# Kernel tuning notes

Measured on AMD Instinct MI355X. Metric: run time of the kernel, lower is better.

Reference implementation:

```python
import jax, jax.numpy as jnp
import numpy as np
from jax import lax

T, B = 256, 64
VOCAB, D_EMBED, D_HIDDEN = 32000, 512, 1024


def setup_inputs() -> dict:
    key = jax.random.key(0)
    k1, k2, k3, k4 = jax.random.split(key, 4)
    x_seq = jax.random.randint(k1, (T, B), 0, VOCAB, dtype=jnp.int64) if jax.config.jax_enable_x64 else jax.random.randint(k1, (T, B), 0, VOCAB, dtype=jnp.int32)
    scale_e = 1.0
    scale_ih = 1.0 / np.sqrt(D_HIDDEN)
    return {
        "x_seq": x_seq,
        "embedding": jax.random.normal(k2, (VOCAB, D_EMBED), dtype=jnp.float32) * scale_e,
        "W_ih": jax.random.normal(k3, (4 * D_HIDDEN, D_EMBED), dtype=jnp.float32) * scale_ih,
        "W_hh": jax.random.normal(k4, (4 * D_HIDDEN, D_HIDDEN), dtype=jnp.float32) * scale_ih,
        "b_ih": jnp.zeros((4 * D_HIDDEN,), dtype=jnp.float32),
        "b_hh": jnp.zeros((4 * D_HIDDEN,), dtype=jnp.float32),
    }


def reference(x_seq, embedding, W_ih, W_hh, b_ih, b_hh):
    # e_seq: [T, B, E]
    e_seq = embedding[x_seq]
    B_ = x_seq.shape[1]
    H = W_hh.shape[1]
    # Precompute input projections for all timesteps in one big GEMM: [T, B, 4H]
    x_gates = jnp.einsum("tbe,ge->tbg", e_seq, W_ih) + b_ih + b_hh

    def step(carry, xg):
        h, c = carry
        gates = xg + h @ W_hh.T  # [B, 4H]
        i, f, g, o = jnp.split(gates, 4, axis=-1)  # PyTorch gate order i,f,g,o
        i = jax.nn.sigmoid(i)
        f = jax.nn.sigmoid(f)
        g = jnp.tanh(g)
        o = jax.nn.sigmoid(o)
        c_new = f * c + i * g
        h_new = o * jnp.tanh(c_new)
        return (h_new, c_new), h_new

    h0 = jnp.zeros((B_, H), dtype=e_seq.dtype)
    c0 = jnp.zeros((B_, H), dtype=e_seq.dtype)
    (h, c), outs = lax.scan(step, (h0, c0), x_gates)
    return outs, h, c
```

## Files before the change

kernel.cpp:

```cpp
#include <hip/hip_runtime.h>
#include <hip/hip_bf16.h>
#include <cstdint>
#include <cstddef>

#define T_STEPS 256
#define BATCH   64
#define DE      512
#define DH      1024
#define NBLK    64

typedef short  bf16x8 __attribute__((ext_vector_type(8)));
typedef float  f32x4  __attribute__((ext_vector_type(4)));
typedef unsigned long long u64;

#define LSBMASK 0x0001000100010001ull

__device__ __forceinline__ unsigned short bf_bits(__hip_bfloat16 h) {
    union { __hip_bfloat16 h; unsigned short u; } x; x.h = h; return x.u;
}
__device__ __forceinline__ float b2f(unsigned short u) {
    union { float f; unsigned v; } x; x.v = ((unsigned)u) << 16; return x.f;
}

__device__ __forceinline__ void async_copy16(const void* gsrc, void* ldst) {
    __builtin_amdgcn_global_load_lds(
        (const __attribute__((address_space(1))) unsigned int*)gsrc,
        (__attribute__((address_space(3))) unsigned int*)ldst,
        16, 0, 0);
}

__device__ __forceinline__ u64 llc_load64(const u64* p) {
    return __hip_atomic_load(p, __ATOMIC_RELAXED, __HIP_MEMORY_SCOPE_AGENT);
}
__device__ __forceinline__ void llc_store16(unsigned short* p, unsigned short v) {
    __hip_atomic_store(p, v, __ATOMIC_RELAXED, __HIP_MEMORY_SCOPE_AGENT);
}

__global__ void k_init(u64* __restrict__ hbuf) {
    int i = blockIdx.x * 256 + threadIdx.x;
    hbuf[i] = (i < 16384) ? 0ull : LSBMASK;
}

__global__ void k_f32_to_bf16(const float* __restrict__ src,
                              __hip_bfloat16* __restrict__ dst, int n8) {
    int i = blockIdx.x * blockDim.x + threadIdx.x;
    if (i >= n8) return;
    const float4* s = (const float4*)src + (size_t)i * 2;
    float4 a = s[0], b = s[1];
    union { unsigned short u[8]; uint4 v; } o;
    o.u[0] = bf_bits(__float2bfloat16(a.x));
    o.u[1] = bf_bits(__float2bfloat16(a.y));
    o.u[2] = bf_bits(__float2bfloat16(a.z));
    o.u[3] = bf_bits(__float2bfloat16(a.w));
    o.u[4] = bf_bits(__float2bfloat16(b.x));
    o.u[5] = bf_bits(__float2bfloat16(b.y));
    o.u[6] = bf_bits(__float2bfloat16(b.z));
    o.u[7] = bf_bits(__float2bfloat16(b.w));
    *((uint4*)dst + i) = o.v;
}

__global__ void k_gather(const int* __restrict__ xs, const float* __restrict__ emb,
                         __hip_bfloat16* __restrict__ e_bf) {
    int tid = blockIdx.x * 256 + threadIdx.x;
    int r = tid >> 6, ch = tid & 63;
    int v = xs[r];
    const float4* s = (const float4*)(emb + (size_t)v * DE + ch * 8);
    float4 a = s[0], b = s[1];
    union { unsigned short u[8]; uint4 v4; } o;
    o.u[0] = bf_bits(__float2bfloat16(a.x));
    o.u[1] = bf_bits(__float2bfloat16(a.y));
    o.u[2] = bf_bits(__float2bfloat16(a.z));
    o.u[3] = bf_bits(__float2bfloat16(a.w));
    o.u[4] = bf_bits(__float2bfloat16(b.x));
    o.u[5] = bf_bits(__float2bfloat16(b.y));
    o.u[6] = bf_bits(__float2bfloat16(b.z));
    o.u[7] = bf_bits(__float2bfloat16(b.w));
    *((uint4*)(e_bf + (size_t)r * DE) + ch) = o.v4;
}

__global__ void k_gemm_xg(const __hip_bfloat16* __restrict__ A,
                          const __hip_bfloat16* __restrict__ Bt,
                          const float* __restrict__ bih, const float* __restrict__ bhh,
                          __hip_bfloat16* __restrict__ xgp) {
    __shared__ __align__(16) __hip_bfloat16 sA[128 * 32];
    __shared__ __align__(16) __hip_bfloat16 sB[128 * 32];
    const int bm = blockIdx.x >> 5;
    const int bn = blockIdx.x & 31;
    const int tid = threadIdx.x;
    const int l = tid & 63, w = tid >> 6;
    const int wm = w >> 1, wn = w & 1;
    const int lrow = l & 15, lq = l >> 4;

    f32x4 acc[4][4] = {};

    for (int kb = 0; kb < 512; kb += 32) {
#pragma unroll
        for (int q = 0; q < 2; ++q) {
            int c = q * 256 + tid;
            int row = c >> 2, seg = c & 3;
            async_copy16(A + (size_t)(bm * 128 + row) * 512 + kb + seg * 8, &sA[c * 8]);
            async_copy16(Bt + (size_t)(bn * 128 + row) * 512 + kb + seg * 8, &sB[c * 8]);
        }
        __syncthreads();
        bf16x8 af[4], bq[4];
#pragma unroll
        for (int mt = 0; mt < 4; ++mt)
            af[mt] = *(const bf16x8*)&sA[(wm * 64 + mt * 16 + lrow) * 32 + lq * 8];
#pragma unroll
        for (int nt = 0; nt < 4; ++nt)
            bq[nt] = *(const bf16x8*)&sB[(wn * 64 + nt * 16 + lrow) * 32 + lq * 8];
#pragma unroll
        for (int mt = 0; mt < 4; ++mt)
#pragma unroll
            for (int nt = 0; nt < 4; ++nt)
                acc[mt][nt] = __builtin_amdgcn_mfma_f32_16x16x32_bf16(
                    af[mt], bq[nt], acc[mt][nt], 0, 0, 0);
        __syncthreads();
    }

#pragma unroll
    for (int nt = 0; nt < 4; ++nt) {
        int n = bn * 128 + wn * 64 + nt * 16 + lrow;
        int g = n >> 10, j = n & 1023, blk = j >> 4, u = j & 15;
        float bias = bih[n] + bhh[n];
#pragma unroll
        for (int mt = 0; mt < 4; ++mt) {
#pragma unroll
            for (int r = 0; r < 4; ++r) {
                int m = bm * 128 + wm * 64 + mt * 16 + lq * 4 + r;
                int t = m >> 6, b = m & 63;
                xgp[(((size_t)(t * NBLK + blk) * 4 + g) * 16 + u) * 64 + b] =
                    __float2bfloat16(acc[mt][nt][r] + bias);
            }
        }
    }
}

__global__ void __launch_bounds__(256) k_lstm(
        const __hip_bfloat16* __restrict__ xgp,
        const __hip_bfloat16* __restrict__ Whh,
        unsigned short* __restrict__ hbuf,
        float* __restrict__ out) {
    __shared__ __hip_bfloat16 sW[65536];
    const int tid = threadIdx.x, l = tid & 63, w = tid >> 6;
    const int lrow = l & 15, lq = l >> 4;
    const int bk = blockIdx.x;

    for (int it = 0; it < 32; ++it) {
        int fi = it * 256 + tid;
        int n = fi & 15, lqq = (fi >> 4) & 3, kc = (fi >> 6) & 31, g = fi >> 11;
        async_copy16(Whh + (size_t)(g * DH + bk * 16 + n) * DH + kc * 32 + lqq * 8,
                     &sW[fi * 8]);
    }
    __syncthreads();

    const int b0 = w * 16 + lq * 4;
    const int abase = (lq * 64 + w * 16 + lrow) * 2;
    const int kg = bk * 16 + lrow;
    const int pbase = ((kg >> 5) * 4 + ((kg & 31) >> 3)) * 512 + (kg & 7);
    float creg[4] = {0.f, 0.f, 0.f, 0.f};

    for (int t = 0; t < T_STEPS; ++t) {
        const u64* hin = (const u64*)hbuf + (size_t)(t & 1) * 16384;
        unsigned short* hout = hbuf + (size_t)((t + 1) & 1) * 65536;
        const u64 expw = ((t >> 1) & 1) ? LSBMASK : 0ull;
        const unsigned short wpar = (unsigned short)(((t + 1) >> 1) & 1);

        const __hip_bfloat16* xgt = xgp + ((size_t)t * NBLK + bk) * 4096;
        ushort4 xv0 = *(const ushort4*)(xgt + (0 * 16 + lrow) * 64 + b0);
        ushort4 xv1 = *(const ushort4*)(xgt + (1 * 16 + lrow) * 64 + b0);
        ushort4 xv2 = *(const ushort4*)(xgt + (2 * 16 + lrow) * 64 + b0);
        ushort4 xv3 = *(const ushort4*)(xgt + (3 * 16 + lrow) * 64 + b0);

        u64 a0[8], a1[8];
#pragma unroll
        for (int p = 0; p < 8; ++p) {
            a0[p] = llc_load64(hin + p * 512 + abase);
            a1[p] = llc_load64(hin + p * 512 + abase + 1);
        }
        f32x4 acc[4] = {};
#pragma unroll
        for (int kc = 0; kc < 32; ++kc) {
            u64 x0 = a0[kc & 7], x1 = a1[kc & 7];
            const u64* p0 = hin + kc * 512 + abase;
            while ((((x0 ^ expw) | (x1 ^ expw)) & LSBMASK) != 0ull) {
                x0 = llc_load64(p0);
                x1 = llc_load64(p0 + 1);
            }
            union { u64 q[2]; bf16x8 v; } A;
            A.q[0] = x0; A.q[1] = x1;
#pragma unroll
            for (int g = 0; g < 4; ++g) {
                bf16x8 bf = *(const bf16x8*)&sW[(((g * 32 + kc) * 4 + lq) * 16 + lrow) * 8];
                acc[g] = __builtin_amdgcn_mfma_f32_16x16x32_bf16(A.v, bf, acc[g], 0, 0, 0);
            }
            if (kc + 8 < 32) {
                a0[kc & 7] = llc_load64(hin + (kc + 8) * 512 + abase);
                a1[kc & 7] = llc_load64(hin + (kc + 8) * 512 + abase + 1);
            }
        }

        const unsigned short* xi = (const unsigned short*)&xv0;
        const unsigned short* xf = (const unsigned short*)&xv1;
        const unsigned short* xg_ = (const unsigned short*)&xv2;
        const unsigned short* xo = (const unsigned short*)&xv3;
#pragma unroll
        for (int r = 0; r < 4; ++r) {
            int b = b0 + r;
            float vi = acc[0][r] + b2f(xi[r]);
            float vf = acc[1][r] + b2f(xf[r]);
            float vg = acc[2][r] + b2f(xg_[r]);
            float vo = acc[3][r] + b2f(xo[r]);
            float ig = 1.0f / (1.0f + __expf(-vi));
            float fg = 1.0f / (1.0f + __expf(-vf));
            float gg = tanhf(vg);
            float og = 1.0f / (1.0f + __expf(-vo));
            float cnew = fg * creg[r] + ig * gg;
            float hnew = og * tanhf(cnew);
            creg[r] = cnew;
            out[((size_t)t * BATCH + b) * DH + kg] = hnew;
            unsigned short hb =
                (unsigned short)((bf_bits(__float2bfloat16(hnew)) & 0xFFFEu) | wpar);
            llc_store16(hout + pbase + b * 8, hb);
            if (t == T_STEPS - 1) {
                out[(size_t)T_STEPS * BATCH * DH + (size_t)b * DH + kg] = hnew;
                out[(size_t)T_STEPS * BATCH * DH + BATCH * DH + (size_t)b * DH + kg] = cnew;
            }
        }
    }
}

extern "C" void kernel_launch(void* const* d_in, const int* in_sizes, int n_in,
                              void* d_out, int out_size, void* d_ws, size_t ws_size,
                              hipStream_t stream) {
    const int*   xs  = (const int*)d_in[0];
    const float* emb = (const float*)d_in[1];
    const float* Wih = (const float*)d_in[2];
    const float* Whh = (const float*)d_in[3];
    const float* bih = (const float*)d_in[4];
    const float* bhh = (const float*)d_in[5];
    float* out = (float*)d_out;
    char*  ws  = (char*)d_ws;

    __hip_bfloat16* Wih_bf = (__hip_bfloat16*)(ws);
    __hip_bfloat16* Whh_bf = (__hip_bfloat16*)(ws + 4194304);
    __hip_bfloat16* e_bf   = (__hip_bfloat16*)(ws + 12582912);
    __hip_bfloat16* xgp    = (__hip_bfloat16*)(ws + 29360128);
    unsigned short* hbuf   = (unsigned short*)(ws + 163577856);

    k_init<<<128, 256, 0, stream>>>((u64*)hbuf);
    k_f32_to_bf16<<<1024, 256, 0, stream>>>(Wih, Wih_bf, 2097152 / 8);
    k_f32_to_bf16<<<2048, 256, 0, stream>>>(Whh, Whh_bf, 4194304 / 8);
    k_gather<<<4096, 256, 0, stream>>>(xs, emb, e_bf);
    k_gemm_xg<<<4096, 256, 0, stream>>>(e_bf, Wih_bf, bih, bhh, xgp);
    k_lstm<<<NBLK, 256, 0, stream>>>(xgp, Whh_bf, hbuf, out);
}
```

Before: 2.524 ms.

## Replace per-element parity-bit polling with per-block flag barrier in LSTM recurrence

Drops the LSB-parity data-embedded synchronisation, where every h element carried a parity bit and was spin-polled. Instead each block publishes a step counter flag after a release fence, and 64 threads poll all flags with sleep before an acquire fence. The MFMA operands are swapped so h is laid out row-major per batch, allowing vectorized float4/u64 stores of outputs and h. The xg layout is changed to match and the next step's xg is prefetched. It also uses a cheaper exp-based tanh. The trade-off is a full grid-wide barrier per step instead of fine-grained, overlapped dependency waiting.

```diff
diff --git a/kernel.cpp b/kernel.cpp
--- a/kernel.cpp
+++ b/kernel.cpp
@@ -13,32 +13,20 @@
 typedef float  f32x4  __attribute__((ext_vector_type(4)));
 typedef unsigned long long u64;
 
-#define LSBMASK 0x0001000100010001ull
-
 __device__ __forceinline__ unsigned short bf_bits(__hip_bfloat16 h) {
     union { __hip_bfloat16 h; unsigned short u; } x; x.h = h; return x.u;
 }
 __device__ __forceinline__ float b2f(unsigned short u) {
     union { float f; unsigned v; } x; x.v = ((unsigned)u) << 16; return x.f;
 }
+__device__ __forceinline__ float sigm(float x) { return 1.0f / (1.0f + __expf(-x)); }
+__device__ __forceinline__ float ftanh(float x) { return 1.0f - 2.0f / (__expf(2.0f * x) + 1.0f); }
 
 __device__ __forceinline__ void async_copy16(const void* gsrc, void* ldst) {
     __builtin_amdgcn_global_load_lds(
         (const __attribute__((address_space(1))) unsigned int*)gsrc,
         (__attribute__((address_space(3))) unsigned int*)ldst,
         16, 0, 0);
-}
-
-__device__ __forceinline__ u64 llc_load64(const u64* p) {
-    return __hip_atomic_load(p, __ATOMIC_RELAXED, __HIP_MEMORY_SCOPE_AGENT);
-}
-__device__ __forceinline__ void llc_store16(unsigned short* p, unsigned short v) {
-    __hip_atomic_store(p, v, __ATOMIC_RELAXED, __HIP_MEMORY_SCOPE_AGENT);
-}
-
-__global__ void k_init(u64* __restrict__ hbuf) {
-    int i = blockIdx.x * 256 + threadIdx.x;
-    hbuf[i] = (i < 16384) ? 0ull : LSBMASK;
 }
 
 __global__ void k_f32_to_bf16(const float* __restrict__ src,
@@ -129,7 +117,7 @@
             for (int r = 0; r < 4; ++r) {
                 int m = bm * 128 + wm * 64 + mt * 16 + lq * 4 + r;
                 int t = m >> 6, b = m & 63;
-                xgp[(((size_t)(t * NBLK + blk) * 4 + g) * 16 + u) * 64 + b] =
+                xgp[(((size_t)(t * NBLK + blk) * 4 + g) * 64 + b) * 16 + u] =
                     __float2bfloat16(acc[mt][nt][r] + bias);
             }
         }
@@ -139,8 +127,9 @@
 __global__ void __launch_bounds__(256) k_lstm(
         const __hip_bfloat16* __restrict__ xgp,
         const __hip_bfloat16* __restrict__ Whh,
-        unsigned short* __restrict__ hbuf,
-        float* __restrict__ out) {
+        __hip_bfloat16* __restrict__ hbuf,
+        float* __restrict__ out,
+        unsigned* __restrict__ flags) {
     __shared__ __hip_bfloat16 sW[65536];
     const int tid = threadIdx.x, l = tid & 63, w = tid >> 6;
     const int lrow = l & 15, lq = l >> 4;
@@ -154,78 +143,88 @@
     }
     __syncthreads();
 
-    const int b0 = w * 16 + lq * 4;
-    const int abase = (lq * 64 + w * 16 + lrow) * 2;
-    const int kg = bk * 16 + lrow;
-    const int pbase = ((kg >> 5) * 4 + ((kg & 31) >> 3)) * 512 + (kg & 7);
+    const int b  = w * 16 + lrow;
+    const int u0 = lq * 4;
+    const int ug = bk * 16 + u0;
     float creg[4] = {0.f, 0.f, 0.f, 0.f};
 
+    ushort4 xv[4];
+#pragma unroll
+    for (int g = 0; g < 4; ++g)
+        xv[g] = *(const ushort4*)(xgp + (((size_t)bk * 4 + g) * 64 + b) * 16 + u0);
+
     for (int t = 0; t < T_STEPS; ++t) {
-        const u64* hin = (const u64*)hbuf + (size_t)(t & 1) * 16384;
-        unsigned short* hout = hbuf + (size_t)((t + 1) & 1) * 65536;
-        const u64 expw = ((t >> 1) & 1) ? LSBMASK : 0ull;
-        const unsigned short wpar = (unsigned short)(((t + 1) >> 1) & 1);
-
-        const __hip_bfloat16* xgt = xgp + ((size_t)t * NBLK + bk) * 4096;
-        ushort4 xv0 = *(const ushort4*)(xgt + (0 * 16 + lrow) * 64 + b0);
-        ushort4 xv1 = *(const ushort4*)(xgt + (1 * 16 + lrow) * 64 + b0);
-        ushort4 xv2 = *(const ushort4*)(xgt + (2 * 16 + lrow) * 64 + b0);
-        ushort4 xv3 = *(const ushort4*)(xgt + (3 * 16 + lrow) * 64 + b0);
-
-        u64 a0[8], a1[8];
-#pragma unroll
-        for (int p = 0; p < 8; ++p) {
-            a0[p] = llc_load64(hin + p * 512 + abase);
-            a1[p] = llc_load64(hin + p * 512 + abase + 1);
-        }
+        if (t > 0) {
+            if (tid < 64) {
+                while (__hip_atomic_load(&flags[tid], __ATOMIC_RELAXED,
+                                         __HIP_MEMORY_SCOPE_AGENT) < (unsigned)t)
+                    __builtin_amdgcn_s_sleep(1);
+            }
+            __syncthreads();
+            __builtin_amdgcn_fence(__ATOMIC_ACQUIRE, "agent");
+        }
+        const __hip_bfloat16* hin = hbuf + (size_t)(t & 1) * 65536 + (size_t)b * DH;
+        __hip_bfloat16* hout = hbuf + (size_t)((t + 1) & 1) * 65536;
+
+        bf16x8 hp[8];
+#pragma unroll
+        for (int p = 0; p < 8; ++p)
+            hp[p] = *(const bf16x8*)(hin + p * 32 + lq * 8);
         f32x4 acc[4] = {};
 #pragma unroll
         for (int kc = 0; kc < 32; ++kc) {
-            u64 x0 = a0[kc & 7], x1 = a1[kc & 7];
-            const u64* p0 = hin + kc * 512 + abase;
-            while ((((x0 ^ expw) | (x1 ^ expw)) & LSBMASK) != 0ull) {
-                x0 = llc_load64(p0);
-                x1 = llc_load64(p0 + 1);
+            bf16x8 hv = hp[kc & 7];
+#pragma unroll
+            for (int g = 0; g < 4; ++g) {
+                bf16x8 af = *(const bf16x8*)&sW[(((g * 32 + kc) * 4 + lq) * 16 + lrow) * 8];
+                acc[g] = __builtin_amdgcn_mfma_f32_16x16x32_bf16(af, hv, acc[g], 0, 0, 0);
             }
-            union { u64 q[2]; bf16x8 v; } A;
-            A.q[0] = x0; A.q[1] = x1;
-#pragma unroll
-            for (int g = 0; g < 4; ++g) {
-                bf16x8 bf = *(const bf16x8*)&sW[(((g * 32 + kc) * 4 + lq) * 16 + lrow) * 8];
-                acc[g] = __builtin_amdgcn_mfma_f32_16x16x32_bf16(A.v, bf, acc[g], 0, 0, 0);
-            }
-            if (kc + 8 < 32) {
-                a0[kc & 7] = llc_load64(hin + (kc + 8) * 512 + abase);
-                a1[kc & 7] = llc_load64(hin + (kc + 8) * 512 + abase + 1);
-            }
-        }
-
-        const unsigned short* xi = (const unsigned short*)&xv0;
-        const unsigned short* xf = (const unsigned short*)&xv1;
-        const unsigned short* xg_ = (const unsigned short*)&xv2;
-        const unsigned short* xo = (const unsigned short*)&xv3;
+            if (kc + 8 < 32)
+                hp[kc & 7] = *(const bf16x8*)(hin + (kc + 8) * 32 + lq * 8);
+        }
+
+        const unsigned short* xi = (const unsigned short*)&xv[0];
+        const unsigned short* xf = (const unsigned short*)&xv[1];
+        const unsigned short* xg = (const unsigned short*)&xv[2];
+        const unsigned short* xo = (const unsigned short*)&xv[3];
+        float4 ov;
+        union { unsigned short s[4]; u64 q; } hp4;
 #pragma unroll
         for (int r = 0; r < 4; ++r) {
-            int b = b0 + r;
             float vi = acc[0][r] + b2f(xi[r]);
             float vf = acc[1][r] + b2f(xf[r]);
-            float vg = acc[2][r] + b2f(xg_[r]);
+            float vg = acc[2][r] + b2f(xg[r]);
             float vo = acc[3][r] + b2f(xo[r]);
-            float ig = 1.0f / (1.0f + __expf(-vi));
-            float fg = 1.0f / (1.0f + __expf(-vf));
-            float gg = tanhf(vg);
-            float og = 1.0f / (1.0f + __expf(-vo));
+            float ig = sigm(vi), fg = sigm(vf), gg = ftanh(vg), og = sigm(vo);
             float cnew = fg * creg[r] + ig * gg;
-            float hnew = og * tanhf(cnew);
+            float hnew = og * ftanh(cnew);
             creg[r] = cnew;
-            out[((size_t)t * BATCH + b) * DH + kg] = hnew;
-            unsigned short hb =
-                (unsigned short)((bf_bits(__float2bfloat16(hnew)) & 0xFFFEu) | wpar);
-            llc_store16(hout + pbase + b * 8, hb);
-            if (t == T_STEPS - 1) {
-                out[(size_t)T_STEPS * BATCH * DH + (size_t)b * DH + kg] = hnew;
-                out[(size_t)T_STEPS * BATCH * DH + BATCH * DH + (size_t)b * DH + kg] = cnew;
-            }
+            (&ov.x)[r] = hnew;
+            hp4.s[r] = bf_bits(__float2bfloat16(hnew));
+        }
+        *(float4*)(out + ((size_t)t * BATCH + b) * DH + ug) = ov;
+        *(u64*)(hout + (size_t)b * DH + ug) = hp4.q;
+        if (t == T_STEPS - 1) {
+            *(float4*)(out + (size_t)T_STEPS * BATCH * DH + (size_t)b * DH + ug) = ov;
+            float4 cv;
+#pragma unroll
+            for (int r = 0; r < 4; ++r) (&cv.x)[r] = creg[r];
+            *(float4*)(out + (size_t)T_STEPS * BATCH * DH + BATCH * DH
+                       + (size_t)b * DH + ug) = cv;
+        }
+        if (t + 1 < T_STEPS) {
+#pragma unroll
+            for (int g = 0; g < 4; ++g)
+                xv[g] = *(const ushort4*)(xgp
+                        + (((size_t)(t + 1) * NBLK + bk) * 4 + g) * 1024
+                        + (size_t)b * 16 + u0);
+        }
+        if (t < T_STEPS - 1) {
+            __builtin_amdgcn_fence(__ATOMIC_RELEASE, "agent");
+            __syncthreads();
+            if (tid == 0)
+                __hip_atomic_store(&flags[bk], (unsigned)(t + 1), __ATOMIC_RELAXED,
+                                   __HIP_MEMORY_SCOPE_AGENT);
         }
     }
 }
@@ -246,12 +245,14 @@
     __hip_bfloat16* Whh_bf = (__hip_bfloat16*)(ws + 4194304);
     __hip_bfloat16* e_bf   = (__hip_bfloat16*)(ws + 12582912);
     __hip_bfloat16* xgp    = (__hip_bfloat16*)(ws + 29360128);
-    unsigned short* hbuf   = (unsigned short*)(ws + 163577856);
-
-    k_init<<<128, 256, 0, stream>>>((u64*)hbuf);
+    __hip_bfloat16* hbuf   = (__hip_bfloat16*)(ws + 163577856);
+    unsigned*       flags  = (unsigned*)(ws + 163840000);
+
+    hipMemsetAsync(hbuf, 0, 131072, stream);
+    hipMemsetAsync(flags, 0, 256, stream);
     k_f32_to_bf16<<<1024, 256, 0, stream>>>(Wih, Wih_bf, 2097152 / 8);
     k_f32_to_bf16<<<2048, 256, 0, stream>>>(Whh, Whh_bf, 4194304 / 8);
     k_gather<<<4096, 256, 0, stream>>>(xs, emb, e_bf);
     k_gemm_xg<<<4096, 256, 0, stream>>>(e_bf, Wih_bf, bih, bhh, xgp);
-    k_lstm<<<NBLK, 256, 0, stream>>>(xgp, Whh_bf, hbuf, out);
-}
+    k_lstm<<<NBLK, 256, 0, stream>>>(xgp, Whh_bf, hbuf, out, flags);
+}
```

Result: slower. 4.732 ms (+87.4%).
